# Kernel optimization log

Hardware: AMD Instinct MI355X
Metric: run time of the kernel (lower is better)

Reference implementation:

```python
import jax, jax.numpy as jnp
import numpy as np

CUTOFF = 15.0
EPS = 1e-08


def _pairwise_dist(x):
    # x: [B, N, 3] -> [B, N, N] euclidean distances (gram trick, no [B,N,N,3] temp)
    x2 = jnp.sum(x * x, axis=-1)                      # [B, N]
    d2 = x2[:, :, None] + x2[:, None, :] - 2.0 * jnp.einsum('bnd,bmd->bnm', x, x)
    d2 = jnp.maximum(d2, 0.0)
    return jnp.sqrt(d2)


def setup_inputs() -> dict:
    key = jax.random.key(0)
    k1, k2 = jax.random.split(key)
    B, N = 8, 2048
    pred_coords = jax.random.normal(k1, (B, N, 3), dtype=jnp.float32)
    true_coords = jax.random.normal(k2, (B, N, 3), dtype=jnp.float32)
    return {"pred_coords": pred_coords, "true_coords": true_coords}


def reference(pred_coords, true_coords):
    pred_d = _pairwise_dist(pred_coords)              # [B, N, N]
    true_d = _pairwise_dist(true_coords)              # [B, N, N]
    local_mask = (true_d < CUTOFF) & (true_d > EPS)   # excludes diagonal
    diff = jnp.abs(pred_d - true_d)
    # piecewise-constant preserved score (0.5/1.0/2.0/4.0 A bins)
    preserved = (
        (diff < 0.5).astype(jnp.float32) * 1.0
        + ((diff >= 0.5) & (diff < 1.0)).astype(jnp.float32) * 0.5
        + ((diff >= 1.0) & (diff < 2.0)).astype(jnp.float32) * 0.25
        + ((diff >= 2.0) & (diff < 4.0)).astype(jnp.float32) * 0.125
    )
    maskf = local_mask.astype(jnp.float32)
    numerator = jnp.sum(preserved * maskf, axis=(-1, -2))    # [B]
    denominator = jnp.maximum(jnp.sum(maskf, axis=(-1, -2)), EPS)
    lddt_per_sample = numerator / denominator
    return jnp.mean(1.0 - lddt_per_sample)
```

## Files before the change

### kernel.cpp

```cpp
#include <hip/hip_runtime.h>
#include <math.h>

constexpr int B  = 8;
constexpr int N  = 2048;
constexpr int TI = 256;
constexpr int TJ = 64;
constexpr int TILES = 144;
constexpr int WPB = TI / 64;

template <bool CHECK>
__device__ __forceinline__ void inner_loop(
    const float* __restrict__ pj,
    const float* __restrict__ tj,
    float pix, float piy, float piz,
    float tix, float tiy, float tiz,
    int k0,
    unsigned& c0, unsigned& c1, unsigned& c2, unsigned& c3, unsigned& cd)
{
    #pragma unroll 4
    for (int j = 0; j < TJ; ++j) {
        float pjx = pj[3 * j + 0], pjy = pj[3 * j + 1], pjz = pj[3 * j + 2];
        float tjx = tj[3 * j + 0], tjy = tj[3 * j + 1], tjz = tj[3 * j + 2];

        float dx = pix - pjx, dy = piy - pjy, dz = piz - pjz;
        float pd2 = fmaf(dx, dx, fmaf(dy, dy, dz * dz));
        float ex = tix - tjx, ey = tiy - tjy, ez = tiz - tjz;
        float td2 = fmaf(ex, ex, fmaf(ey, ey, ez * ez));

        unsigned long long m = __ballot(td2 < 225.0f);
        if (CHECK) {
            int kw = k0 + j;
            unsigned long long mji =
                (kw >= 64) ? ~0ull : ((kw <= 0) ? 0ull : ((1ull << kw) - 1ull));
            m &= mji;
        }

        float diff = fabsf(__builtin_amdgcn_sqrtf(pd2) - __builtin_amdgcn_sqrtf(td2));

        c0 += __popcll(m & __ballot(diff < 0.5f));
        c1 += __popcll(m & __ballot(diff < 1.0f));
        c2 += __popcll(m & __ballot(diff < 2.0f));
        c3 += __popcll(m & __ballot(diff < 4.0f));
        cd += __popcll(m);
    }
}

__global__ __launch_bounds__(TI) void lddt_partial(
    const float* __restrict__ pred,
    const float* __restrict__ truec,
    float2* __restrict__ part)
{
    const int b = blockIdx.y;
    int r = blockIdx.x, a = 0;
    while (r >= 32 - 4 * a) { r -= 32 - 4 * a; ++a; }
    const int c = 4 * a + r;
    const int i0 = a * TI;
    const int j0 = c * TJ;
    const int t = threadIdx.x;
    const int wave = t >> 6;

    const int i = i0 + t;
    const float* pi = pred  + ((size_t)b * N + i) * 3;
    const float* ti = truec + ((size_t)b * N + i) * 3;
    const float pix = pi[0], piy = pi[1], piz = pi[2];
    const float tix = ti[0], tiy = ti[1], tiz = ti[2];

    const float* pj = pred  + ((size_t)b * N + j0) * 3;
    const float* tj = truec + ((size_t)b * N + j0) * 3;

    unsigned c0 = 0, c1 = 0, c2 = 0, c3 = 0, cd = 0;

    if (c >= 4 * a + 4) {
        inner_loop<false>(pj, tj, pix, piy, piz, tix, tiy, tiz, 0,
                          c0, c1, c2, c3, cd);
    } else {
        const int k0 = j0 - (i0 + 64 * wave);
        inner_loop<true>(pj, tj, pix, piy, piz, tix, tiy, tiz, k0,
                         c0, c1, c2, c3, cd);
    }

    if ((t & 63) == 0) {
        float n = 0.5f * (float)c0 + 0.25f * (float)c1
                + 0.125f * (float)c2 + 0.125f * (float)c3;
        part[(size_t)b * (TILES * WPB) + blockIdx.x * WPB + wave] =
            make_float2(n, (float)cd);
    }
}

__global__ __launch_bounds__(512) void lddt_reduce(
    const float2* __restrict__ part,
    float* __restrict__ out)
{
    constexpr int SLOTS = TILES * WPB;
    const int t = threadIdx.x;
    const int w = t >> 6;
    const int l = t & 63;

    float n = 0.0f, d = 0.0f;
    for (int s = l; s < SLOTS; s += 64) {
        float2 v = part[(size_t)w * SLOTS + s];
        n += v.x;
        d += v.y;
    }
    for (int off = 32; off > 0; off >>= 1) {
        n += __shfl_down(n, off, 64);
        d += __shfl_down(d, off, 64);
    }

    __shared__ float acc[B];
    if (l == 0) acc[w] = 1.0f - n / fmaxf(d, 1e-8f);
    __syncthreads();

    if (t == 0) {
        float s = 0.0f;
        #pragma unroll
        for (int b = 0; b < B; ++b) s += acc[b];
        out[0] = s / (float)B;
    }
}

extern "C" void kernel_launch(void* const* d_in, const int* in_sizes, int n_in,
                              void* d_out, int out_size, void* d_ws, size_t ws_size,
                              hipStream_t stream)
{
    const float* pred  = (const float*)d_in[0];
    const float* truec = (const float*)d_in[1];
    float* out   = (float*)d_out;
    float2* part = (float2*)d_ws;

    dim3 grid(TILES, B);
    lddt_partial<<<grid, TI, 0, stream>>>(pred, truec, part);
    lddt_reduce<<<1, 512, 0, stream>>>(part, out);
}
```

Baseline: 76.84 us.

## Stage j-coordinates in LDS with gram-form distances and select-based masking

Preloads each block's 64 j-points into shared memory as float4 (-2x,-2y,-2z,|x|^2), so the inner loop computes squared distances with three FMAs instead of subtract-and-square. This replaces the repeated strided global loads. The triangular mask becomes a per-lane compare folded into a select rather than a 64-bit mask build, and the unroll factor rises to 8. The cost is an added __syncthreads, plus possible cancellation error from the gram form that could flip bin decisions near thresholds.

```diff
diff --git a/kernel.cpp b/kernel.cpp
--- a/kernel.cpp
+++ b/kernel.cpp
@@ -7,41 +7,37 @@
 constexpr int TJ = 64;
 constexpr int TILES = 144;
 constexpr int WPB = TI / 64;
+constexpr int SLOTS = TILES * WPB;
 
 template <bool CHECK>
 __device__ __forceinline__ void inner_loop(
-    const float* __restrict__ pj,
-    const float* __restrict__ tj,
-    float pix, float piy, float piz,
-    float tix, float tiy, float tiz,
-    int k0,
+    const float4* __restrict__ sjp,
+    const float4* __restrict__ sjt,
+    float pix, float piy, float piz, float x2pi,
+    float tix, float tiy, float tiz, float x2ti,
+    int k0, int lane,
     unsigned& c0, unsigned& c1, unsigned& c2, unsigned& c3, unsigned& cd)
 {
-    #pragma unroll 4
+    #pragma unroll 8
     for (int j = 0; j < TJ; ++j) {
-        float pjx = pj[3 * j + 0], pjy = pj[3 * j + 1], pjz = pj[3 * j + 2];
-        float tjx = tj[3 * j + 0], tjy = tj[3 * j + 1], tjz = tj[3 * j + 2];
+        float4 P = sjp[j];
+        float4 T = sjt[j];
+        float pd2 = fmaf(P.x, pix, fmaf(P.y, piy, fmaf(P.z, piz, x2pi + P.w)));
+        float td2 = fmaf(T.x, tix, fmaf(T.y, tiy, fmaf(T.z, tiz, x2ti + T.w)));
+        pd2 = fmaxf(pd2, 0.0f);
+        td2 = fmaxf(td2, 0.0f);
 
-        float dx = pix - pjx, dy = piy - pjy, dz = piz - pjz;
-        float pd2 = fmaf(dx, dx, fmaf(dy, dy, dz * dz));
-        float ex = tix - tjx, ey = tiy - tjy, ez = tiz - tjz;
-        float td2 = fmaf(ex, ex, fmaf(ey, ey, ez * ez));
+        bool keep = td2 < 225.0f;
+        if (CHECK) keep = keep && (lane < k0 + j);
 
-        unsigned long long m = __ballot(td2 < 225.0f);
-        if (CHECK) {
-            int kw = k0 + j;
-            unsigned long long mji =
-                (kw >= 64) ? ~0ull : ((kw <= 0) ? 0ull : ((1ull << kw) - 1ull));
-            m &= mji;
-        }
+        float diff = __builtin_amdgcn_sqrtf(pd2) - __builtin_amdgcn_sqrtf(td2);
+        float dg = keep ? fabsf(diff) : 1e9f;
 
-        float diff = fabsf(__builtin_amdgcn_sqrtf(pd2) - __builtin_amdgcn_sqrtf(td2));
-
-        c0 += __popcll(m & __ballot(diff < 0.5f));
-        c1 += __popcll(m & __ballot(diff < 1.0f));
-        c2 += __popcll(m & __ballot(diff < 2.0f));
-        c3 += __popcll(m & __ballot(diff < 4.0f));
-        cd += __popcll(m);
+        cd += __popcll(__ballot(keep));
+        c0 += __popcll(__ballot(dg < 0.5f));
+        c1 += __popcll(__ballot(dg < 1.0f));
+        c2 += __popcll(__ballot(dg < 2.0f));
+        c3 += __popcll(__ballot(dg < 4.0f));
     }
 }
 
@@ -58,31 +54,46 @@
     const int j0 = c * TJ;
     const int t = threadIdx.x;
     const int wave = t >> 6;
+    const int lane = t & 63;
+
+    __shared__ float4 sjp[TJ];
+    __shared__ float4 sjt[TJ];
+
+    if (t < TJ) {
+        const float* pp = pred  + ((size_t)b * N + j0 + t) * 3;
+        const float* tp = truec + ((size_t)b * N + j0 + t) * 3;
+        float px = pp[0], py = pp[1], pz = pp[2];
+        float tx = tp[0], ty = tp[1], tz = tp[2];
+        sjp[t] = make_float4(-2.0f * px, -2.0f * py, -2.0f * pz,
+                             fmaf(px, px, fmaf(py, py, pz * pz)));
+        sjt[t] = make_float4(-2.0f * tx, -2.0f * ty, -2.0f * tz,
+                             fmaf(tx, tx, fmaf(ty, ty, tz * tz)));
+    }
 
     const int i = i0 + t;
     const float* pi = pred  + ((size_t)b * N + i) * 3;
     const float* ti = truec + ((size_t)b * N + i) * 3;
     const float pix = pi[0], piy = pi[1], piz = pi[2];
     const float tix = ti[0], tiy = ti[1], tiz = ti[2];
-
-    const float* pj = pred  + ((size_t)b * N + j0) * 3;
-    const float* tj = truec + ((size_t)b * N + j0) * 3;
+    const float x2pi = fmaf(pix, pix, fmaf(piy, piy, piz * piz));
+    const float x2ti = fmaf(tix, tix, fmaf(tiy, tiy, tiz * tiz));
+    __syncthreads();
 
     unsigned c0 = 0, c1 = 0, c2 = 0, c3 = 0, cd = 0;
 
     if (c >= 4 * a + 4) {
-        inner_loop<false>(pj, tj, pix, piy, piz, tix, tiy, tiz, 0,
-                          c0, c1, c2, c3, cd);
+        inner_loop<false>(sjp, sjt, pix, piy, piz, x2pi, tix, tiy, tiz, x2ti,
+                          0, lane, c0, c1, c2, c3, cd);
     } else {
         const int k0 = j0 - (i0 + 64 * wave);
-        inner_loop<true>(pj, tj, pix, piy, piz, tix, tiy, tiz, k0,
-                         c0, c1, c2, c3, cd);
+        inner_loop<true>(sjp, sjt, pix, piy, piz, x2pi, tix, tiy, tiz, x2ti,
+                         k0, lane, c0, c1, c2, c3, cd);
     }
 
-    if ((t & 63) == 0) {
+    if (lane == 0) {
         float n = 0.5f * (float)c0 + 0.25f * (float)c1
                 + 0.125f * (float)c2 + 0.125f * (float)c3;
-        part[(size_t)b * (TILES * WPB) + blockIdx.x * WPB + wave] =
+        part[(size_t)b * SLOTS + blockIdx.x * WPB + wave] =
             make_float2(n, (float)cd);
     }
 }
@@ -91,7 +102,6 @@
     const float2* __restrict__ part,
     float* __restrict__ out)
 {
-    constexpr int SLOTS = TILES * WPB;
     const int t = threadIdx.x;
     const int w = t >> 6;
     const int l = t & 63;
```

After: 72.48 us. -5.7%, faster.
